# Kernel optimization log

Measured on AMD Instinct MI355X. Metric: run time of the kernel, lower is better.

Reference implementation:

```python
import jax, jax.numpy as jnp
import numpy as np

N_NODES = 50000
N_EDGES = 1600000
N_GRAPHS = 512
HID = 64


def _mlp_params(key, din, dout, scale=0.1):
    k1, k2, k3 = jax.random.split(key, 3)
    return (
        jax.random.normal(k1, (din, HID), jnp.float32) * scale, jnp.zeros((HID,), jnp.float32),
        jax.random.normal(k2, (HID, HID), jnp.float32) * scale, jnp.zeros((HID,), jnp.float32),
        jax.random.normal(k3, (HID, dout), jnp.float32) * scale, jnp.zeros((dout,), jnp.float32),
    )


def _mlp(x, w1, b1, w2, b2, w3, b3, out_act=None):
    h = jax.nn.relu(x @ w1 + b1)
    h = jax.nn.relu(h @ w2 + b2)
    o = h @ w3 + b3
    return o if out_act is None else out_act(o)


def setup_inputs() -> dict:
    key = jax.random.key(0)
    ks = jax.random.split(key, 8)
    nf = jax.random.normal(ks[0], (N_NODES, 1), jnp.float32)
    ef = jax.random.normal(ks[1], (N_EDGES, 1), jnp.float32)
    src = jax.random.randint(ks[2], (N_EDGES,), 0, N_NODES)
    dst = jax.random.randint(ks[3], (N_EDGES,), 0, N_NODES)
    graph_id = jnp.sort(jax.random.randint(ks[4], (N_NODES,), 0, N_GRAPHS))
    e_w1, e_b1, e_w2, e_b2, e_w3, e_b3 = _mlp_params(ks[5], 3, 1)   # edge model: [src_nf, dst_nf, ef] -> msg
    n_w1, n_b1, n_w2, n_b2, n_w3, n_b3 = _mlp_params(ks[6], 2, 1)   # node model: [nf, agg] -> unf
    m_w1, m_b1, m_w2, m_b2, m_w3, m_b3 = _mlp_params(ks[7], 1, 1)   # node-wise MLP with Sigmoid out_act
    return dict(nf=nf, ef=ef, src=src, dst=dst, graph_id=graph_id,
                e_w1=e_w1, e_b1=e_b1, e_w2=e_w2, e_b2=e_b2, e_w3=e_w3, e_b3=e_b3,
                n_w1=n_w1, n_b1=n_b1, n_w2=n_w2, n_b2=n_b2, n_w3=n_w3, n_b3=n_b3,
                m_w1=m_w1, m_b1=m_b1, m_w2=m_w2, m_b2=m_b2, m_w3=m_w3, m_b3=m_b3)


def reference(nf, ef, src, dst, graph_id,
              e_w1, e_b1, e_w2, e_b2, e_w3, e_b3,
              n_w1, n_b1, n_w2, n_b2, n_w3, n_b3,
              m_w1, m_b1, m_w2, m_b2, m_w3, m_b3):
    # MPNN layer: message on edges, sum-aggregate to dst nodes, node update
    em_in = jnp.concatenate([nf[src], nf[dst], ef], axis=-1)          # [E, 3]
    msg = _mlp(em_in, e_w1, e_b1, e_w2, e_b2, e_w3, e_b3)             # [E, 1]
    agg = jax.ops.segment_sum(msg, dst, num_segments=N_NODES)        # [N, 1]
    unf = _mlp(jnp.concatenate([nf, agg], axis=-1),
               n_w1, n_b1, n_w2, n_b2, n_w3, n_b3)                    # [N, 1]
    # node-wise MLP with Sigmoid output activation
    node_out = _mlp(unf, m_w1, m_b1, m_w2, m_b2, m_w3, m_b3,
                    out_act=jax.nn.sigmoid)                           # [N, 1]
    # sum readout per graph, then final sigmoid
    rd = jax.ops.segment_sum(node_out, graph_id, num_segments=N_GRAPHS)  # [G, 1]
    return jax.nn.sigmoid(rd)
```

## Files before the change

kernel.cpp:

```cpp
#include <hip/hip_runtime.h>
#include <math.h>

#define HID 64
#define BKT_SHIFT 13
#define BKT_RANGE 8192
#define CCHUNK 32

typedef __attribute__((ext_vector_type(8))) short short8;
typedef __attribute__((ext_vector_type(4))) float f32x4;
typedef unsigned long long ull;

union FragU {
    uint4 q;
    short8 v;
    uint32_t u[4];
};

__device__ __forceinline__ uint32_t cvt_pk_bf16(float lo, float hi) {
    uint32_t r;
    asm("v_cvt_pk_bf16_f32 %0, %1, %2" : "=v"(r) : "v"(lo), "v"(hi));
    return r;
}
__device__ __forceinline__ unsigned short bf16_of(float v) {
    return (unsigned short)(cvt_pk_bf16(v, 0.f) & 0xFFFFu);
}

__global__ void prep_kernel(
    const float* __restrict__ w1,  const float* __restrict__ b1,  const float* __restrict__ w2,
    const float* __restrict__ nw1, const float* __restrict__ nb1, const float* __restrict__ nw2,
    const float* __restrict__ mw1, const float* __restrict__ mb1, const float* __restrict__ mw2,
    unsigned short* __restrict__ w1x,  unsigned short* __restrict__ w2T,
    unsigned short* __restrict__ nw1x, unsigned short* __restrict__ nw2T,
    unsigned short* __restrict__ mw1x, unsigned short* __restrict__ mw2T)
{
    int t = blockIdx.x * 256 + threadIdx.x;
    if (t < 4096) {
        int j = t >> 6, k = t & 63;
        w2T [t] = bf16_of(w2 [k * HID + j]);
        nw2T[t] = bf16_of(nw2[k * HID + j]);
        mw2T[t] = bf16_of(mw2[k * HID + j]);
    }
    if (t < 512) {
        int j = t >> 3, k = t & 7;
        float ve = k == 0 ? w1[j] : k == 1 ? w1[HID + j] : k == 2 ? w1[2 * HID + j] : k == 3 ? b1[j] : 0.f;
        float vn = k == 0 ? nw1[j] : k == 1 ? nw1[HID + j] : k == 2 ? nb1[j] : 0.f;
        float vm = k == 0 ? mw1[j] : k == 1 ? mb1[j] : 0.f;
        w1x [t] = bf16_of(ve);
        nw1x[t] = bf16_of(vn);
        mw1x[t] = bf16_of(vm);
    }
}

__global__ __launch_bounds__(256, 2) void edge_mfma7_kernel(
    const float* __restrict__ nf, const float* __restrict__ ef,
    const int* __restrict__ src, const int* __restrict__ dst,
    const unsigned short* __restrict__ w1x, const unsigned short* __restrict__ w2T,
    const float* __restrict__ b2, const float* __restrict__ w3, const float* __restrict__ b3,
    uint2* __restrict__ recs, ull* __restrict__ offs,
    float* __restrict__ aggFb, int E, int B, int nbatch, int mode)
{
    __shared__ uint2 tile[4][2][16][16];

    const int tid  = threadIdx.x;
    const int lane = tid & 63;
    const int wid  = tid >> 6;
    const int g    = lane >> 4;
    const int eL   = lane & 15;

    FragU af1[4];
#pragma unroll
    for (int t = 0; t < 4; ++t) {
        uint4 q = *(const uint4*)&w1x[(t * 16 + eL) * 8];
        af1[t].q = (g == 0) ? q : make_uint4(0, 0, 0, 0);
    }
    FragU af2[4][2];
#pragma unroll
    for (int t = 0; t < 4; ++t)
#pragma unroll
        for (int h = 0; h < 2; ++h)
            af2[t][h].q = *(const uint4*)&w2T[(t * 16 + eL) * 64 + h * 32 + g * 8];

    f32x4 b2v4[4], w3v4[4];
#pragma unroll
    for (int t = 0; t < 4; ++t) {
        int j = t * 16 + g * 4;
        b2v4[t] = *(const f32x4*)&b2[j];
        w3v4[t] = *(const f32x4*)&w3[j];
    }
    const float b3c = b3[0];

    int bi   = blockIdx.x;
    if (bi >= nbatch) return;
    int eidx = bi * 256 + tid;
    int ei   = eidx < E ? eidx : E - 1;
    int dcur = dst[ei];
    float a  = nf[src[ei]];
    float b  = nf[dcur];
    float c  = ef[ei];

    for (;;) {
        const int nbi   = bi + gridDim.x;
        const bool hn   = nbi < nbatch;
        const int neidx = hn ? nbi * 256 + tid : eidx;
        const int nei   = neidx < E ? neidx : E - 1;
        const int ns    = src[nei];
        const int nd    = dst[nei];
        const float ncf = ef[nei];

        float na = 0.f, nb = 0.f;
        float mymsg = 0.f;

#pragma unroll
        for (int ph = 0; ph < 2; ++ph) {
#pragma unroll
            for (int ss = 0; ss < 2; ++ss) {
                const int s = 2 * ph + ss;
                float av = __shfl(a, s * 16 + eL);
                float bv = __shfl(b, s * 16 + eL);
                float cv = __shfl(c, s * 16 + eL);
                FragU bin;
                bin.u[0] = (g == 0) ? cvt_pk_bf16(av, bv) : 0u;
                bin.u[1] = (g == 0) ? cvt_pk_bf16(cv, 1.0f) : 0u;
                bin.u[2] = 0u; bin.u[3] = 0u;
#pragma unroll
                for (int t = 0; t < 4; ++t) {
                    f32x4 h4 = __builtin_amdgcn_mfma_f32_16x16x32_bf16(
                        af1[t].v, bin.v, (f32x4){0.f, 0.f, 0.f, 0.f}, 0, 0, 0);
                    uint32_t p0 = cvt_pk_bf16(fmaxf(h4[0], 0.f), fmaxf(h4[1], 0.f));
                    uint32_t p1 = cvt_pk_bf16(fmaxf(h4[2], 0.f), fmaxf(h4[3], 0.f));
                    tile[wid][ss][eL][(4 * t + g) ^ ((eL & 7) << 1)] = make_uint2(p0, p1);
                }
            }

            if (ph == 0) {
                na = nf[ns];
                nb = nf[nd];
            }

            __builtin_amdgcn_s_setprio(1);
#pragma unroll
            for (int ss = 0; ss < 2; ++ss) {
                const int s = 2 * ph + ss;
                const uint4* row = (const uint4*)&tile[wid][ss][eL][0];
                FragU bf0, bf1;
                bf0.q = row[(g)     ^ (eL & 7)];
                bf1.q = row[(4 + g) ^ (eL & 7)];

                float q0, q1, q2, q3;
                {
                    f32x4 ac = __builtin_amdgcn_mfma_f32_16x16x32_bf16(af2[0][0].v, bf0.v, b2v4[0], 0, 0, 0);
                    ac = __builtin_amdgcn_mfma_f32_16x16x32_bf16(af2[0][1].v, bf1.v, ac, 0, 0, 0);
                    q0 = fmaxf(ac[0], 0.f) * w3v4[0][0];
                    q0 = fmaf(fmaxf(ac[1], 0.f), w3v4[0][1], q0);
                    q0 = fmaf(fmaxf(ac[2], 0.f), w3v4[0][2], q0);
                    q0 = fmaf(fmaxf(ac[3], 0.f), w3v4[0][3], q0);
                }
                {
                    f32x4 ac = __builtin_amdgcn_mfma_f32_16x16x32_bf16(af2[1][0].v, bf0.v, b2v4[1], 0, 0, 0);
                    ac = __builtin_amdgcn_mfma_f32_16x16x32_bf16(af2[1][1].v, bf1.v, ac, 0, 0, 0);
                    q1 = fmaxf(ac[0], 0.f) * w3v4[1][0];
                    q1 = fmaf(fmaxf(ac[1], 0.f), w3v4[1][1], q1);
                    q1 = fmaf(fmaxf(ac[2], 0.f), w3v4[1][2], q1);
                    q1 = fmaf(fmaxf(ac[3], 0.f), w3v4[1][3], q1);
                }
                {
                    f32x4 ac = __builtin_amdgcn_mfma_f32_16x16x32_bf16(af2[2][0].v, bf0.v, b2v4[2], 0, 0, 0);
                    ac = __builtin_amdgcn_mfma_f32_16x16x32_bf16(af2[2][1].v, bf1.v, ac, 0, 0, 0);
                    q2 = fmaxf(ac[0], 0.f) * w3v4[2][0];
                    q2 = fmaf(fmaxf(ac[1], 0.f), w3v4[2][1], q2);
                    q2 = fmaf(fmaxf(ac[2], 0.f), w3v4[2][2], q2);
                    q2 = fmaf(fmaxf(ac[3], 0.f), w3v4[2][3], q2);
                }
                {
                    f32x4 ac = __builtin_amdgcn_mfma_f32_16x16x32_bf16(af2[3][0].v, bf0.v, b2v4[3], 0, 0, 0);
                    ac = __builtin_amdgcn_mfma_f32_16x16x32_bf16(af2[3][1].v, bf1.v, ac, 0, 0, 0);
                    q3 = fmaxf(ac[0], 0.f) * w3v4[3][0];
                    q3 = fmaf(fmaxf(ac[1], 0.f), w3v4[3][1], q3);
                    q3 = fmaf(fmaxf(ac[2], 0.f), w3v4[3][2], q3);
                    q3 = fmaf(fmaxf(ac[3], 0.f), w3v4[3][3], q3);
                }
                float p = (q0 + q1) + (q2 + q3);
                p += __shfl_xor(p, 16);
                p += __shfl_xor(p, 32);
                if (s == g) mymsg = p + b3c;
            }
            __builtin_amdgcn_s_setprio(0);
        }

        const bool valid = eidx < E;

        if (mode == 1) {
            if (valid) atomicAdd(&aggFb[dcur], mymsg);
        } else {
            const int bkt = dcur >> BKT_SHIFT;
            const ull lt = (1ull << lane) - 1;
            int myslot = 0;
            int off = 0;
            uint32_t pack_lo = 0, pack_hi = 0;
            for (int bb = 0; bb < B; ++bb) {
                if (bb < 4) pack_lo |= (uint32_t)off << (8 * bb);
                else        pack_hi |= (uint32_t)off << (8 * (bb - 4));
                ull m = __ballot(valid && bkt == bb);
                if (valid && bkt == bb) myslot = off + (int)__popcll(m & lt);
                off += (int)__popcll(m);
            }
            pack_hi |= (uint32_t)off << 24;

            const size_t wgl = (size_t)bi * 4 + wid;
            if (valid) recs[wgl * 64 + myslot] = make_uint2((uint32_t)dcur, __float_as_uint(mymsg));
            if (lane == 0) offs[wgl] = ((ull)pack_hi << 32) | (ull)pack_lo;
        }

        if (!hn) break;
        bi = nbi; eidx = neidx; ei = nei;
        a = na; b = nb; c = ncf; dcur = nd;
    }
}

__global__ __launch_bounds__(256) void bucket_accum_kernel(
    const uint2* __restrict__ recs, const ull* __restrict__ offs,
    float* __restrict__ partial, float* __restrict__ rd, int G, int NW, int B)
{
    __shared__ float acc[BKT_RANGE];

    const int b = blockIdx.x / CCHUNK;
    const int c = blockIdx.x % CCHUNK;

    if (blockIdx.x == 0)
        for (int i = threadIdx.x; i < G; i += 256) rd[i] = 0.f;

    for (int i = threadIdx.x; i < BKT_RANGE; i += 256) acc[i] = 0.f;
    __syncthreads();

    const int wpc = (NW + CCHUNK - 1) / CCHUNK;
    const int w0 = c * wpc;
    const int w1 = (w0 + wpc < NW) ? w0 + wpc : NW;
    const int nb = b + 1;
    const int base_node = b << BKT_SHIFT;

    for (int w = w0 + threadIdx.x; w < w1; w += 256) {
        ull ov = offs[w];
        uint32_t lo = (uint32_t)ov, hi = (uint32_t)(ov >> 32);
        int ob = (int)(((b  < 4) ? (lo >> (8 * b))  : (hi >> (8 * (b  - 4)))) & 0xFF);
        int oe = (int)(((nb < 4) ? (lo >> (8 * nb)) : (hi >> (8 * (nb - 4)))) & 0xFF);
        const uint2* rb = recs + (size_t)w * 64;
        for (int r = ob; r < oe; ++r) {
            uint2 rec = rb[r];
            atomicAdd(&acc[(int)rec.x - base_node], __uint_as_float(rec.y));
        }
    }
    __syncthreads();

    float* pb = partial + ((size_t)b * CCHUNK + c) * BKT_RANGE;
    for (int i = threadIdx.x; i < BKT_RANGE; i += 256) pb[i] = acc[i];
}

__global__ __launch_bounds__(256, 2) void node_mfma4_kernel(
    const float* __restrict__ nf, const float* __restrict__ partial,
    const float* __restrict__ aggFb, int nplanes,
    const int* __restrict__ gid,
    const unsigned short* __restrict__ nw1x, const unsigned short* __restrict__ nw2T,
    const float* __restrict__ nb2, const float* __restrict__ nw3, const float* __restrict__ nb3,
    const unsigned short* __restrict__ mw1x, const unsigned short* __restrict__ mw2T,
    const float* __restrict__ mb2, const float* __restrict__ mw3, const float* __restrict__ mb3,
    float* __restrict__ rd, int N)
{
    __shared__ uint2 tile[4][4][16][16];

    const int tid  = threadIdx.x;
    const int lane = tid & 63;
    const int wid  = tid >> 6;
    const int g    = lane >> 4;
    const int eL   = lane & 15;

    const int idx = blockIdx.x * 256 + tid;
    const int i   = idx < N ? idx : N - 1;
    const float x0 = nf[i];
    const int   gg = gid[i];

    float x1;
    if (nplanes == 1) {
        x1 = aggFb[i];
    } else {
        int bb = i >> BKT_SHIFT, nl = i & (BKT_RANGE - 1);
        const float* p = partial + (size_t)bb * CCHUNK * BKT_RANGE + nl;
        x1 = 0.f;
#pragma unroll 8
        for (int c = 0; c < CCHUNK; ++c) x1 += p[(size_t)c * BKT_RANGE];
    }

    float myunf = 0.f, o = 0.f;

    {
        FragU af1[4], af2[4][2];
        f32x4 b2v4[4], w3v4[4];
#pragma unroll
        for (int t = 0; t < 4; ++t) {
            uint4 q = *(const uint4*)&nw1x[(t * 16 + eL) * 8];
            af1[t].q = (g == 0) ? q : make_uint4(0, 0, 0, 0);
#pragma unroll
            for (int h = 0; h < 2; ++h)
                af2[t][h].q = *(const uint4*)&nw2T[(t * 16 + eL) * 64 + h * 32 + g * 8];
            int j = t * 16 + g * 4;
            b2v4[t] = *(const f32x4*)&nb2[j];
            w3v4[t] = *(const f32x4*)&nw3[j];
        }

#pragma unroll
        for (int s = 0; s < 4; ++s) {
            float av = __shfl(x0, s * 16 + eL);
            float bv = __shfl(x1, s * 16 + eL);
            FragU bin;
            bin.u[0] = (g == 0) ? cvt_pk_bf16(av, bv) : 0u;
            bin.u[1] = (g == 0) ? cvt_pk_bf16(1.0f, 0.f) : 0u;
            bin.u[2] = 0u; bin.u[3] = 0u;
#pragma unroll
            for (int t = 0; t < 4; ++t) {
                f32x4 h4 = __builtin_amdgcn_mfma_f32_16x16x32_bf16(
                    af1[t].v, bin.v, (f32x4){0.f, 0.f, 0.f, 0.f}, 0, 0, 0);
                uint32_t p0 = cvt_pk_bf16(fmaxf(h4[0], 0.f), fmaxf(h4[1], 0.f));
                uint32_t p1 = cvt_pk_bf16(fmaxf(h4[2], 0.f), fmaxf(h4[3], 0.f));
                tile[wid][s][eL][(4 * t + g) ^ ((eL & 7) << 1)] = make_uint2(p0, p1);
            }
        }
#pragma unroll
        for (int s = 0; s < 4; ++s) {
            const uint4* row = (const uint4*)&tile[wid][s][eL][0];
            FragU bf0, bf1;
            bf0.q = row[(g)     ^ (eL & 7)];
            bf1.q = row[(4 + g) ^ (eL & 7)];
            float p = 0.f;
#pragma unroll
            for (int t = 0; t < 4; ++t) {
                f32x4 ac = __builtin_amdgcn_mfma_f32_16x16x32_bf16(af2[t][0].v, bf0.v, b2v4[t], 0, 0, 0);
                ac = __builtin_amdgcn_mfma_f32_16x16x32_bf16(af2[t][1].v, bf1.v, ac, 0, 0, 0);
                p = fmaf(fmaxf(ac[0], 0.f), w3v4[t][0], p);
                p = fmaf(fmaxf(ac[1], 0.f), w3v4[t][1], p);
                p = fmaf(fmaxf(ac[2], 0.f), w3v4[t][2], p);
                p = fmaf(fmaxf(ac[3], 0.f), w3v4[t][3], p);
            }
            p += __shfl_xor(p, 16);
            p += __shfl_xor(p, 32);
            if (s == g) myunf = p + nb3[0];
        }
    }

    {
        FragU af1[4], af2[4][2];
        f32x4 b2v4[4], w3v4[4];
#pragma unroll
        for (int t = 0; t < 4; ++t) {
            uint4 q = *(const uint4*)&mw1x[(t * 16 + eL) * 8];
            af1[t].q = (g == 0) ? q : make_uint4(0, 0, 0, 0);
#pragma unroll
            for (int h = 0; h < 2; ++h)
                af2[t][h].q = *(const uint4*)&mw2T[(t * 16 + eL) * 64 + h * 32 + g * 8];
            int j = t * 16 + g * 4;
            b2v4[t] = *(const f32x4*)&mb2[j];
            w3v4[t] = *(const f32x4*)&mw3[j];
        }

#pragma unroll
        for (int s = 0; s < 4; ++s) {
            float uv = __shfl(myunf, s * 16 + eL);
            FragU bin;
            bin.u[0] = (g == 0) ? cvt_pk_bf16(uv, 1.0f) : 0u;
            bin.u[1] = 0u; bin.u[2] = 0u; bin.u[3] = 0u;
#pragma unroll
            for (int t = 0; t < 4; ++t) {
                f32x4 h4 = __builtin_amdgcn_mfma_f32_16x16x32_bf16(
                    af1[t].v, bin.v, (f32x4){0.f, 0.f, 0.f, 0.f}, 0, 0, 0);
                uint32_t p0 = cvt_pk_bf16(fmaxf(h4[0], 0.f), fmaxf(h4[1], 0.f));
                uint32_t p1 = cvt_pk_bf16(fmaxf(h4[2], 0.f), fmaxf(h4[3], 0.f));
                tile[wid][s][eL][(4 * t + g) ^ ((eL & 7) << 1)] = make_uint2(p0, p1);
            }
        }
#pragma unroll
        for (int s = 0; s < 4; ++s) {
            const uint4* row = (const uint4*)&tile[wid][s][eL][0];
            FragU bf0, bf1;
            bf0.q = row[(g)     ^ (eL & 7)];
            bf1.q = row[(4 + g) ^ (eL & 7)];
            float p = 0.f;
#pragma unroll
            for (int t = 0; t < 4; ++t) {
                f32x4 ac = __builtin_amdgcn_mfma_f32_16x16x32_bf16(af2[t][0].v, bf0.v, b2v4[t], 0, 0, 0);
                ac = __builtin_amdgcn_mfma_f32_16x16x32_bf16(af2[t][1].v, bf1.v, ac, 0, 0, 0);
                p = fmaf(fmaxf(ac[0], 0.f), w3v4[t][0], p);
                p = fmaf(fmaxf(ac[1], 0.f), w3v4[t][1], p);
                p = fmaf(fmaxf(ac[2], 0.f), w3v4[t][2], p);
                p = fmaf(fmaxf(ac[3], 0.f), w3v4[t][3], p);
            }
            p += __shfl_xor(p, 16);
            p += __shfl_xor(p, 32);
            if (s == g) o = p + mb3[0];
        }
    }

    const float node_out = 1.0f / (1.0f + expf(-o));

    {
        const bool ok = idx < N;
        float v = ok ? node_out : 0.0f;
        int ggv = gg;
#pragma unroll
        for (int d = 1; d < 64; d <<= 1) {
            float vup = __shfl_up(v, d);
            int   gup = __shfl_up(ggv, d);
            if (lane >= d && gup == ggv) v += vup;
        }
        int gdn = __shfl_down(ggv, 1);
        bool tail = (lane == 63) || (gdn != ggv);
        if (tail)
            atomicAdd(&rd[ggv], v);
    }
}

__global__ void readout_kernel(const float* __restrict__ rd,
                               float* __restrict__ out, int G)
{
    int g = blockIdx.x * blockDim.x + threadIdx.x;
    if (g < G) out[g] = 1.0f / (1.0f + expf(-rd[g]));
}

extern "C" void kernel_launch(void* const* d_in, const int* in_sizes, int n_in,
                              void* d_out, int out_size, void* d_ws, size_t ws_size,
                              hipStream_t stream)
{
    const float* nf  = (const float*)d_in[0];
    const float* ef  = (const float*)d_in[1];
    const int*   src = (const int*)  d_in[2];
    const int*   dst = (const int*)  d_in[3];
    const int*   gid = (const int*)  d_in[4];

    const float* e_w1 = (const float*)d_in[5];
    const float* e_b1 = (const float*)d_in[6];
    const float* e_w2 = (const float*)d_in[7];
    const float* e_b2 = (const float*)d_in[8];
    const float* e_w3 = (const float*)d_in[9];
    const float* e_b3 = (const float*)d_in[10];

    const float* n_w1 = (const float*)d_in[11];
    const float* n_b1 = (const float*)d_in[12];
    const float* n_w2 = (const float*)d_in[13];
    const float* n_b2 = (const float*)d_in[14];
    const float* n_w3 = (const float*)d_in[15];
    const float* n_b3 = (const float*)d_in[16];

    const float* m_w1 = (const float*)d_in[17];
    const float* m_b1 = (const float*)d_in[18];
    const float* m_w2 = (const float*)d_in[19];
    const float* m_b2 = (const float*)d_in[20];
    const float* m_w3 = (const float*)d_in[21];
    const float* m_b3 = (const float*)d_in[22];

    const int N = in_sizes[0];
    const int E = in_sizes[2];
    const int G = out_size;

    const int nbatch = (E + 255) / 256;
    const int NW = (E + 63) / 64;
    const int B  = (N + BKT_RANGE - 1) / BKT_RANGE;

    size_t wts_b  = 32 * 1024;
    size_t recs_b = (size_t)NW * 64 * sizeof(uint2);
    size_t offs_b = (size_t)NW * sizeof(ull);
    size_t part_b = (size_t)B * CCHUNK * BKT_RANGE * sizeof(float);
    size_t need   = wts_b + recs_b + offs_b + part_b + (size_t)G * sizeof(float);
    bool bucketok = (B <= 8) && (need <= ws_size);

    char* wp = (char*)d_ws;
    unsigned short* w1x  = (unsigned short*)(wp);
    unsigned short* nw1x = (unsigned short*)(wp + 1024);
    unsigned short* mw1x = (unsigned short*)(wp + 2048);
    unsigned short* w2T  = (unsigned short*)(wp + 4096);
    unsigned short* nw2T = (unsigned short*)(wp + 4096 + 8192);
    unsigned short* mw2T = (unsigned short*)(wp + 4096 + 16384);

    float* out = (float*)d_out;

    prep_kernel<<<16, 256, 0, stream>>>(
        e_w1, e_b1, e_w2, n_w1, n_b1, n_w2, m_w1, m_b1, m_w2,
        w1x, w2T, nw1x, nw2T, mw1x, mw2T);

    int egrid = nbatch < 2048 ? nbatch : 2048;

    if (bucketok) {
        uint2* recs    = (uint2*)(wp + wts_b);
        ull*   offs    = (ull*)(wp + wts_b + recs_b);
        float* partial = (float*)(wp + wts_b + recs_b + offs_b);
        float* rd      = (float*)(wp + wts_b + recs_b + offs_b + part_b);

        edge_mfma7_kernel<<<egrid, 256, 0, stream>>>(
            nf, ef, src, dst, w1x, w2T, e_b2, e_w3, e_b3,
            recs, offs, nullptr, E, B, nbatch, 0);

        bucket_accum_kernel<<<B * CCHUNK, 256, 0, stream>>>(
            recs, offs, partial, rd, G, NW, B);

        node_mfma4_kernel<<<(N + 255) / 256, 256, 0, stream>>>(
            nf, partial, nullptr, CCHUNK, gid,
            nw1x, nw2T, n_b2, n_w3, n_b3,
            mw1x, mw2T, m_b2, m_w3, m_b3,
            rd, N);

        readout_kernel<<<(G + 255) / 256, 256, 0, stream>>>(rd, out, G);
    } else {
        float* agg = (float*)(wp + wts_b);
        float* rd  = agg + N;

        hipMemsetAsync(agg, 0, ((size_t)N + G) * sizeof(float), stream);

        edge_mfma7_kernel<<<egrid, 256, 0, stream>>>(
            nf, ef, src, dst, w1x, w2T, e_b2, e_w3, e_b3,
            nullptr, nullptr, agg, E, B, nbatch, 1);

        node_mfma4_kernel<<<(N + 255) / 256, 256, 0, stream>>>(
            nf, nullptr, agg, 1, gid,
            nw1x, nw2T, n_b2, n_w3, n_b3,
            mw1x, mw2T, m_b2, m_w3, m_b3,
            rd, N);

        readout_kernel<<<(G + 255) / 256, 256, 0, stream>>>(rd, out, G);
    }
}
```

Before: 78.41 us.

## Remove prep and readout launches by converting weights in-kernel and fusing readout

Result: faster. 71.94 us, median of 2 (-8.2%).

```diff
diff --git a/kernel.cpp b/kernel.cpp
--- a/kernel.cpp
+++ b/kernel.cpp
@@ -21,45 +21,17 @@
     asm("v_cvt_pk_bf16_f32 %0, %1, %2" : "=v"(r) : "v"(lo), "v"(hi));
     return r;
 }
-__device__ __forceinline__ unsigned short bf16_of(float v) {
-    return (unsigned short)(cvt_pk_bf16(v, 0.f) & 0xFFFFu);
-}
-
-__global__ void prep_kernel(
-    const float* __restrict__ w1,  const float* __restrict__ b1,  const float* __restrict__ w2,
-    const float* __restrict__ nw1, const float* __restrict__ nb1, const float* __restrict__ nw2,
-    const float* __restrict__ mw1, const float* __restrict__ mb1, const float* __restrict__ mw2,
-    unsigned short* __restrict__ w1x,  unsigned short* __restrict__ w2T,
-    unsigned short* __restrict__ nw1x, unsigned short* __restrict__ nw2T,
-    unsigned short* __restrict__ mw1x, unsigned short* __restrict__ mw2T)
-{
-    int t = blockIdx.x * 256 + threadIdx.x;
-    if (t < 4096) {
-        int j = t >> 6, k = t & 63;
-        w2T [t] = bf16_of(w2 [k * HID + j]);
-        nw2T[t] = bf16_of(nw2[k * HID + j]);
-        mw2T[t] = bf16_of(mw2[k * HID + j]);
-    }
-    if (t < 512) {
-        int j = t >> 3, k = t & 7;
-        float ve = k == 0 ? w1[j] : k == 1 ? w1[HID + j] : k == 2 ? w1[2 * HID + j] : k == 3 ? b1[j] : 0.f;
-        float vn = k == 0 ? nw1[j] : k == 1 ? nw1[HID + j] : k == 2 ? nb1[j] : 0.f;
-        float vm = k == 0 ? mw1[j] : k == 1 ? mb1[j] : 0.f;
-        w1x [t] = bf16_of(ve);
-        nw1x[t] = bf16_of(vn);
-        mw1x[t] = bf16_of(vm);
-    }
-}
-
-__global__ __launch_bounds__(256, 2) void edge_mfma7_kernel(
+
+__global__ __launch_bounds__(256, 2) void edge_mfma8_kernel(
     const float* __restrict__ nf, const float* __restrict__ ef,
     const int* __restrict__ src, const int* __restrict__ dst,
-    const unsigned short* __restrict__ w1x, const unsigned short* __restrict__ w2T,
-    const float* __restrict__ b2, const float* __restrict__ w3, const float* __restrict__ b3,
+    const float* __restrict__ w1, const float* __restrict__ b1,
+    const float* __restrict__ w2, const float* __restrict__ b2,
+    const float* __restrict__ w3, const float* __restrict__ b3,
     uint2* __restrict__ recs, ull* __restrict__ offs,
     float* __restrict__ aggFb, int E, int B, int nbatch, int mode)
 {
-    __shared__ uint2 tile[4][2][16][16];
+    __shared__ uint2 tile[4][4][16][16];
 
     const int tid  = threadIdx.x;
     const int lane = tid & 63;
@@ -70,16 +42,24 @@
     FragU af1[4];
 #pragma unroll
     for (int t = 0; t < 4; ++t) {
-        uint4 q = *(const uint4*)&w1x[(t * 16 + eL) * 8];
-        af1[t].q = (g == 0) ? q : make_uint4(0, 0, 0, 0);
+        int j = t * 16 + eL;
+        uint32_t u0 = cvt_pk_bf16(w1[j], w1[HID + j]);
+        uint32_t u1 = cvt_pk_bf16(w1[2 * HID + j], b1[j]);
+        af1[t].u[0] = (g == 0) ? u0 : 0u;
+        af1[t].u[1] = (g == 0) ? u1 : 0u;
+        af1[t].u[2] = 0u; af1[t].u[3] = 0u;
     }
     FragU af2[4][2];
 #pragma unroll
     for (int t = 0; t < 4; ++t)
 #pragma unroll
         for (int h = 0; h < 2; ++h)
-            af2[t][h].q = *(const uint4*)&w2T[(t * 16 + eL) * 64 + h * 32 + g * 8];
-
+#pragma unroll
+            for (int e2 = 0; e2 < 4; ++e2) {
+                int k0 = h * 32 + g * 8 + 2 * e2;
+                int j  = t * 16 + eL;
+                af2[t][h].u[e2] = cvt_pk_bf16(w2[k0 * HID + j], w2[(k0 + 1) * HID + j]);
+            }
     f32x4 b2v4[4], w3v4[4];
 #pragma unroll
     for (int t = 0; t < 4; ++t) {
@@ -97,6 +77,8 @@
     float a  = nf[src[ei]];
     float b  = nf[dcur];
     float c  = ef[ei];
+    uint32_t pkab = cvt_pk_bf16(a, b);
+    uint32_t pkc1 = cvt_pk_bf16(c, 1.0f);
 
     for (;;) {
         const int nbi   = bi + gridDim.x;
@@ -107,84 +89,73 @@
         const int nd    = dst[nei];
         const float ncf = ef[nei];
 
-        float na = 0.f, nb = 0.f;
+#pragma unroll
+        for (int s = 0; s < 4; ++s) {
+            int sel = s * 16 + eL;
+            uint32_t u0 = (uint32_t)__shfl((int)pkab, sel);
+            uint32_t u1 = (uint32_t)__shfl((int)pkc1, sel);
+            FragU bin;
+            bin.u[0] = (g == 0) ? u0 : 0u;
+            bin.u[1] = (g == 0) ? u1 : 0u;
+            bin.u[2] = 0u; bin.u[3] = 0u;
+#pragma unroll
+            for (int t = 0; t < 4; ++t) {
+                f32x4 h4 = __builtin_amdgcn_mfma_f32_16x16x32_bf16(
+                    af1[t].v, bin.v, (f32x4){0.f, 0.f, 0.f, 0.f}, 0, 0, 0);
+                uint32_t p0 = cvt_pk_bf16(fmaxf(h4[0], 0.f), fmaxf(h4[1], 0.f));
+                uint32_t p1 = cvt_pk_bf16(fmaxf(h4[2], 0.f), fmaxf(h4[3], 0.f));
+                tile[wid][s][eL][(4 * t + g) ^ ((eL & 7) << 1)] = make_uint2(p0, p1);
+            }
+        }
+
+        const float na = nf[ns];
+        const float nb = nf[nd];
+
         float mymsg = 0.f;
-
-#pragma unroll
-        for (int ph = 0; ph < 2; ++ph) {
-#pragma unroll
-            for (int ss = 0; ss < 2; ++ss) {
-                const int s = 2 * ph + ss;
-                float av = __shfl(a, s * 16 + eL);
-                float bv = __shfl(b, s * 16 + eL);
-                float cv = __shfl(c, s * 16 + eL);
-                FragU bin;
-                bin.u[0] = (g == 0) ? cvt_pk_bf16(av, bv) : 0u;
-                bin.u[1] = (g == 0) ? cvt_pk_bf16(cv, 1.0f) : 0u;
-                bin.u[2] = 0u; bin.u[3] = 0u;
-#pragma unroll
-                for (int t = 0; t < 4; ++t) {
-                    f32x4 h4 = __builtin_amdgcn_mfma_f32_16x16x32_bf16(
-                        af1[t].v, bin.v, (f32x4){0.f, 0.f, 0.f, 0.f}, 0, 0, 0);
-                    uint32_t p0 = cvt_pk_bf16(fmaxf(h4[0], 0.f), fmaxf(h4[1], 0.f));
-                    uint32_t p1 = cvt_pk_bf16(fmaxf(h4[2], 0.f), fmaxf(h4[3], 0.f));
-                    tile[wid][ss][eL][(4 * t + g) ^ ((eL & 7) << 1)] = make_uint2(p0, p1);
-                }
-            }
-
-            if (ph == 0) {
-                na = nf[ns];
-                nb = nf[nd];
-            }
-
-            __builtin_amdgcn_s_setprio(1);
-#pragma unroll
-            for (int ss = 0; ss < 2; ++ss) {
-                const int s = 2 * ph + ss;
-                const uint4* row = (const uint4*)&tile[wid][ss][eL][0];
-                FragU bf0, bf1;
-                bf0.q = row[(g)     ^ (eL & 7)];
-                bf1.q = row[(4 + g) ^ (eL & 7)];
-
-                float q0, q1, q2, q3;
-                {
-                    f32x4 ac = __builtin_amdgcn_mfma_f32_16x16x32_bf16(af2[0][0].v, bf0.v, b2v4[0], 0, 0, 0);
-                    ac = __builtin_amdgcn_mfma_f32_16x16x32_bf16(af2[0][1].v, bf1.v, ac, 0, 0, 0);
-                    q0 = fmaxf(ac[0], 0.f) * w3v4[0][0];
-                    q0 = fmaf(fmaxf(ac[1], 0.f), w3v4[0][1], q0);
-                    q0 = fmaf(fmaxf(ac[2], 0.f), w3v4[0][2], q0);
-                    q0 = fmaf(fmaxf(ac[3], 0.f), w3v4[0][3], q0);
-                }
-                {
-                    f32x4 ac = __builtin_amdgcn_mfma_f32_16x16x32_bf16(af2[1][0].v, bf0.v, b2v4[1], 0, 0, 0);
-                    ac = __builtin_amdgcn_mfma_f32_16x16x32_bf16(af2[1][1].v, bf1.v, ac, 0, 0, 0);
-                    q1 = fmaxf(ac[0], 0.f) * w3v4[1][0];
-                    q1 = fmaf(fmaxf(ac[1], 0.f), w3v4[1][1], q1);
-                    q1 = fmaf(fmaxf(ac[2], 0.f), w3v4[1][2], q1);
-                    q1 = fmaf(fmaxf(ac[3], 0.f), w3v4[1][3], q1);
-                }
-                {
-                    f32x4 ac = __builtin_amdgcn_mfma_f32_16x16x32_bf16(af2[2][0].v, bf0.v, b2v4[2], 0, 0, 0);
-                    ac = __builtin_amdgcn_mfma_f32_16x16x32_bf16(af2[2][1].v, bf1.v, ac, 0, 0, 0);
-                    q2 = fmaxf(ac[0], 0.f) * w3v4[2][0];
-                    q2 = fmaf(fmaxf(ac[1], 0.f), w3v4[2][1], q2);
-                    q2 = fmaf(fmaxf(ac[2], 0.f), w3v4[2][2], q2);
-                    q2 = fmaf(fmaxf(ac[3], 0.f), w3v4[2][3], q2);
-                }
-                {
-                    f32x4 ac = __builtin_amdgcn_mfma_f32_16x16x32_bf16(af2[3][0].v, bf0.v, b2v4[3], 0, 0, 0);
-                    ac = __builtin_amdgcn_mfma_f32_16x16x32_bf16(af2[3][1].v, bf1.v, ac, 0, 0, 0);
-                    q3 = fmaxf(ac[0], 0.f) * w3v4[3][0];
-                    q3 = fmaf(fmaxf(ac[1], 0.f), w3v4[3][1], q3);
-                    q3 = fmaf(fmaxf(ac[2], 0.f), w3v4[3][2], q3);
-                    q3 = fmaf(fmaxf(ac[3], 0.f), w3v4[3][3], q3);
-                }
-                float p = (q0 + q1) + (q2 + q3);
-                p += __shfl_xor(p, 16);
-                p += __shfl_xor(p, 32);
-                if (s == g) mymsg = p + b3c;
-            }
-            __builtin_amdgcn_s_setprio(0);
+#pragma unroll
+        for (int s = 0; s < 4; ++s) {
+            const uint4* row = (const uint4*)&tile[wid][s][eL][0];
+            FragU bf0, bf1;
+            bf0.q = row[(g)     ^ (eL & 7)];
+            bf1.q = row[(4 + g) ^ (eL & 7)];
+
+            float q0, q1, q2, q3;
+            {
+                f32x4 ac = __builtin_amdgcn_mfma_f32_16x16x32_bf16(af2[0][0].v, bf0.v, b2v4[0], 0, 0, 0);
+                ac = __builtin_amdgcn_mfma_f32_16x16x32_bf16(af2[0][1].v, bf1.v, ac, 0, 0, 0);
+                q0 = fmaxf(ac[0], 0.f) * w3v4[0][0];
+                q0 = fmaf(fmaxf(ac[1], 0.f), w3v4[0][1], q0);
+                q0 = fmaf(fmaxf(ac[2], 0.f), w3v4[0][2], q0);
+                q0 = fmaf(fmaxf(ac[3], 0.f), w3v4[0][3], q0);
+            }
+            {
+                f32x4 ac = __builtin_amdgcn_mfma_f32_16x16x32_bf16(af2[1][0].v, bf0.v, b2v4[1], 0, 0, 0);
+                ac = __builtin_amdgcn_mfma_f32_16x16x32_bf16(af2[1][1].v, bf1.v, ac, 0, 0, 0);
+                q1 = fmaxf(ac[0], 0.f) * w3v4[1][0];
+                q1 = fmaf(fmaxf(ac[1], 0.f), w3v4[1][1], q1);
+                q1 = fmaf(fmaxf(ac[2], 0.f), w3v4[1][2], q1);
+                q1 = fmaf(fmaxf(ac[3], 0.f), w3v4[1][3], q1);
+            }
+            {
+                f32x4 ac = __builtin_amdgcn_mfma_f32_16x16x32_bf16(af2[2][0].v, bf0.v, b2v4[2], 0, 0, 0);
+                ac = __builtin_amdgcn_mfma_f32_16x16x32_bf16(af2[2][1].v, bf1.v, ac, 0, 0, 0);
+                q2 = fmaxf(ac[0], 0.f) * w3v4[2][0];
+                q2 = fmaf(fmaxf(ac[1], 0.f), w3v4[2][1], q2);
+                q2 = fmaf(fmaxf(ac[2], 0.f), w3v4[2][2], q2);
+                q2 = fmaf(fmaxf(ac[3], 0.f), w3v4[2][3], q2);
+            }
+            {
+                f32x4 ac = __builtin_amdgcn_mfma_f32_16x16x32_bf16(af2[3][0].v, bf0.v, b2v4[3], 0, 0, 0);
+                ac = __builtin_amdgcn_mfma_f32_16x16x32_bf16(af2[3][1].v, bf1.v, ac, 0, 0, 0);
+                q3 = fmaxf(ac[0], 0.f) * w3v4[3][0];
+                q3 = fmaf(fmaxf(ac[1], 0.f), w3v4[3][1], q3);
+                q3 = fmaf(fmaxf(ac[2], 0.f), w3v4[3][2], q3);
+                q3 = fmaf(fmaxf(ac[3], 0.f), w3v4[3][3], q3);
+            }
+            float p = (q0 + q1) + (q2 + q3);
+            p += __shfl_xor(p, 16);
+            p += __shfl_xor(p, 32);
+            if (s == g) mymsg = p + b3c;
         }
 
         const bool valid = eidx < E;
@@ -212,22 +183,27 @@
         }
 
         if (!hn) break;
-        bi = nbi; eidx = neidx; ei = nei;
-        a = na; b = nb; c = ncf; dcur = nd;
+        bi = nbi; eidx = neidx;
+        pkab = cvt_pk_bf16(na, nb);
+        pkc1 = cvt_pk_bf16(ncf, 1.0f);
+        dcur = nd;
     }
 }
 
 __global__ __launch_bounds__(256) void bucket_accum_kernel(
     const uint2* __restrict__ recs, const ull* __restrict__ offs,
-    float* __restrict__ partial, float* __restrict__ rd, int G, int NW, int B)
+    float* __restrict__ partial, float* __restrict__ rd, unsigned* __restrict__ ctr,
+    int G, int NW, int B)
 {
     __shared__ float acc[BKT_RANGE];
 
     const int b = blockIdx.x / CCHUNK;
     const int c = blockIdx.x % CCHUNK;
 
-    if (blockIdx.x == 0)
+    if (blockIdx.x == 0) {
         for (int i = threadIdx.x; i < G; i += 256) rd[i] = 0.f;
+        if (threadIdx.x == 0) *ctr = 0u;
+    }
 
     for (int i = threadIdx.x; i < BKT_RANGE; i += 256) acc[i] = 0.f;
     __syncthreads();
@@ -255,17 +231,21 @@
     for (int i = threadIdx.x; i < BKT_RANGE; i += 256) pb[i] = acc[i];
 }
 
-__global__ __launch_bounds__(256, 2) void node_mfma4_kernel(
+__global__ __launch_bounds__(256, 2) void node_mfma5_kernel(
     const float* __restrict__ nf, const float* __restrict__ partial,
     const float* __restrict__ aggFb, int nplanes,
     const int* __restrict__ gid,
-    const unsigned short* __restrict__ nw1x, const unsigned short* __restrict__ nw2T,
-    const float* __restrict__ nb2, const float* __restrict__ nw3, const float* __restrict__ nb3,
-    const unsigned short* __restrict__ mw1x, const unsigned short* __restrict__ mw2T,
-    const float* __restrict__ mb2, const float* __restrict__ mw3, const float* __restrict__ mb3,
-    float* __restrict__ rd, int N)
+    const float* __restrict__ nw1, const float* __restrict__ nb1,
+    const float* __restrict__ nw2, const float* __restrict__ nb2,
+    const float* __restrict__ nw3, const float* __restrict__ nb3,
+    const float* __restrict__ mw1, const float* __restrict__ mb1,
+    const float* __restrict__ mw2, const float* __restrict__ mb2,
+    const float* __restrict__ mw3, const float* __restrict__ mb3,
+    float* __restrict__ rd, float* __restrict__ outp, unsigned* __restrict__ ctr,
+    int N, int G)
 {
     __shared__ uint2 tile[4][4][16][16];
+    __shared__ int lastflag;
 
     const int tid  = threadIdx.x;
     const int lane = tid & 63;
@@ -296,23 +276,33 @@
         f32x4 b2v4[4], w3v4[4];
 #pragma unroll
         for (int t = 0; t < 4; ++t) {
-            uint4 q = *(const uint4*)&nw1x[(t * 16 + eL) * 8];
-            af1[t].q = (g == 0) ? q : make_uint4(0, 0, 0, 0);
+            int j = t * 16 + eL;
+            uint32_t u0 = cvt_pk_bf16(nw1[j], nw1[HID + j]);
+            uint32_t u1 = cvt_pk_bf16(nb1[j], 0.f);
+            af1[t].u[0] = (g == 0) ? u0 : 0u;
+            af1[t].u[1] = (g == 0) ? u1 : 0u;
+            af1[t].u[2] = 0u; af1[t].u[3] = 0u;
 #pragma unroll
             for (int h = 0; h < 2; ++h)
-                af2[t][h].q = *(const uint4*)&nw2T[(t * 16 + eL) * 64 + h * 32 + g * 8];
-            int j = t * 16 + g * 4;
-            b2v4[t] = *(const f32x4*)&nb2[j];
-            w3v4[t] = *(const f32x4*)&nw3[j];
-        }
+#pragma unroll
+                for (int e2 = 0; e2 < 4; ++e2) {
+                    int k0 = h * 32 + g * 8 + 2 * e2;
+                    af2[t][h].u[e2] = cvt_pk_bf16(nw2[k0 * HID + j], nw2[(k0 + 1) * HID + j]);
+                }
+            int j4 = t * 16 + g * 4;
+            b2v4[t] = *(const f32x4*)&nb2[j4];
+            w3v4[t] = *(const f32x4*)&nw3[j4];
+        }
+        uint32_t pk01 = cvt_pk_bf16(x0, x1);
+        uint32_t pkb  = cvt_pk_bf16(1.0f, 0.f);
 
 #pragma unroll
         for (int s = 0; s < 4; ++s) {
-            float av = __shfl(x0, s * 16 + eL);
-            float bv = __shfl(x1, s * 16 + eL);
+            int sel = s * 16 + eL;
+            uint32_t u0 = (uint32_t)__shfl((int)pk01, sel);
             FragU bin;
-            bin.u[0] = (g == 0) ? cvt_pk_bf16(av, bv) : 0u;
-            bin.u[1] = (g == 0) ? cvt_pk_bf16(1.0f, 0.f) : 0u;
+            bin.u[0] = (g == 0) ? u0 : 0u;
+            bin.u[1] = (g == 0) ? pkb : 0u;
             bin.u[2] = 0u; bin.u[3] = 0u;
 #pragma unroll
             for (int t = 0; t < 4; ++t) {
@@ -350,14 +340,20 @@
         f32x4 b2v4[4], w3v4[4];
 #pragma unroll
         for (int t = 0; t < 4; ++t) {
-            uint4 q = *(const uint4*)&mw1x[(t * 16 + eL) * 8];
-            af1[t].q = (g == 0) ? q : make_uint4(0, 0, 0, 0);
+            int j = t * 16 + eL;
+            uint32_t u0 = cvt_pk_bf16(mw1[j], mb1[j]);
+            af1[t].u[0] = (g == 0) ? u0 : 0u;
+            af1[t].u[1] = 0u; af1[t].u[2] = 0u; af1[t].u[3] = 0u;
 #pragma unroll
             for (int h = 0; h < 2; ++h)
-                af2[t][h].q = *(const uint4*)&mw2T[(t * 16 + eL) * 64 + h * 32 + g * 8];
-            int j = t * 16 + g * 4;
-            b2v4[t] = *(const f32x4*)&mb2[j];
-            w3v4[t] = *(const f32x4*)&mw3[j];
+#pragma unroll
+                for (int e2 = 0; e2 < 4; ++e2) {
+                    int k0 = h * 32 + g * 8 + 2 * e2;
+                    af2[t][h].u[e2] = cvt_pk_bf16(mw2[k0 * HID + j], mw2[(k0 + 1) * HID + j]);
+                }
+            int j4 = t * 16 + g * 4;
+            b2v4[t] = *(const f32x4*)&mb2[j4];
+            w3v4[t] = *(const f32x4*)&mw3[j4];
         }
 
 #pragma unroll
@@ -413,6 +409,20 @@
         bool tail = (lane == 63) || (gdn != ggv);
         if (tail)
             atomicAdd(&rd[ggv], v);
+    }
+
+    if (ctr) {
+        if (tid == 0) {
+            __threadfence();
+            unsigned v = atomicAdd(ctr, 1u);
+            lastflag = (v == (unsigned)(gridDim.x - 1)) ? 1 : 0;
+        }
+        __syncthreads();
+        if (lastflag) {
+            __threadfence();
+            for (int q = tid; q < G; q += 256)
+                outp[q] = 1.0f / (1.0f + expf(-rd[q]));
+        }
     }
 }
 
@@ -462,65 +472,52 @@
     const int NW = (E + 63) / 64;
     const int B  = (N + BKT_RANGE - 1) / BKT_RANGE;
 
-    size_t wts_b  = 32 * 1024;
     size_t recs_b = (size_t)NW * 64 * sizeof(uint2);
     size_t offs_b = (size_t)NW * sizeof(ull);
     size_t part_b = (size_t)B * CCHUNK * BKT_RANGE * sizeof(float);
-    size_t need   = wts_b + recs_b + offs_b + part_b + (size_t)G * sizeof(float);
+    size_t need   = recs_b + offs_b + part_b + (size_t)G * sizeof(float) + 64;
     bool bucketok = (B <= 8) && (need <= ws_size);
 
     char* wp = (char*)d_ws;
-    unsigned short* w1x  = (unsigned short*)(wp);
-    unsigned short* nw1x = (unsigned short*)(wp + 1024);
-    unsigned short* mw1x = (unsigned short*)(wp + 2048);
-    unsigned short* w2T  = (unsigned short*)(wp + 4096);
-    unsigned short* nw2T = (unsigned short*)(wp + 4096 + 8192);
-    unsigned short* mw2T = (unsigned short*)(wp + 4096 + 16384);
-
     float* out = (float*)d_out;
 
-    prep_kernel<<<16, 256, 0, stream>>>(
-        e_w1, e_b1, e_w2, n_w1, n_b1, n_w2, m_w1, m_b1, m_w2,
-        w1x, w2T, nw1x, nw2T, mw1x, mw2T);
-
-    int egrid = nbatch < 2048 ? nbatch : 2048;
+    int egrid = nbatch < 1024 ? nbatch : 1024;
 
     if (bucketok) {
-        uint2* recs    = (uint2*)(wp + wts_b);
-        ull*   offs    = (ull*)(wp + wts_b + recs_b);
-        float* partial = (float*)(wp + wts_b + recs_b + offs_b);
-        float* rd      = (float*)(wp + wts_b + recs_b + offs_b + part_b);
-
-        edge_mfma7_kernel<<<egrid, 256, 0, stream>>>(
-            nf, ef, src, dst, w1x, w2T, e_b2, e_w3, e_b3,
+        uint2*    recs    = (uint2*)wp;
+        ull*      offs    = (ull*)(wp + recs_b);
+        float*    partial = (float*)(wp + recs_b + offs_b);
+        float*    rd      = (float*)(wp + recs_b + offs_b + part_b);
+        unsigned* ctr     = (unsigned*)(wp + recs_b + offs_b + part_b + (size_t)G * sizeof(float));
+
+        edge_mfma8_kernel<<<egrid, 256, 0, stream>>>(
+            nf, ef, src, dst, e_w1, e_b1, e_w2, e_b2, e_w3, e_b3,
             recs, offs, nullptr, E, B, nbatch, 0);
 
         bucket_accum_kernel<<<B * CCHUNK, 256, 0, stream>>>(
-            recs, offs, partial, rd, G, NW, B);
-
-        node_mfma4_kernel<<<(N + 255) / 256, 256, 0, stream>>>(
+            recs, offs, partial, rd, ctr, G, NW, B);
+
+        node_mfma5_kernel<<<(N + 255) / 256, 256, 0, stream>>>(
             nf, partial, nullptr, CCHUNK, gid,
-            nw1x, nw2T, n_b2, n_w3, n_b3,
-            mw1x, mw2T, m_b2, m_w3, m_b3,
-            rd, N);
+            n_w1, n_b1, n_w2, n_b2, n_w3, n_b3,
+            m_w1, m_b1, m_w2, m_b2, m_w3, m_b3,
+            rd, out, ctr, N, G);
+    } else {
+        float* agg = (float*)wp;
+        float* rd  = agg + N;
+
+        hipMemsetAsync(agg, 0, ((size_t)N + G) * sizeof(float), stream);
+
+        edge_mfma8_kernel<<<egrid, 256, 0, stream>>>(
+            nf, ef, src, dst, e_w1, e_b1, e_w2, e_b2, e_w3, e_b3,
+            nullptr, nullptr, agg, E, B, nbatch, 1);
+
+        node_mfma5_kernel<<<(N + 255) / 256, 256, 0, stream>>>(
+            nf, nullptr, agg, 1, gid,
+            n_w1, n_b1, n_w2, n_b2, n_w3, n_b3,
+            m_w1, m_b1, m_w2, m_b2, m_w3, m_b3,
+            rd, out, nullptr, N, G);
 
         readout_kernel<<<(G + 255) / 256, 256, 0, stream>>>(rd, out, G);
-    } else {
-        float* agg = (float*)(wp + wts_b);
-        float* rd  = agg + N;
-
-        hipMemsetAsync(agg, 0, ((size_t)N + G) * sizeof(float), stream);
-
-        edge_mfma7_kernel<<<egrid, 256, 0, stream>>>(
-            nf, ef, src, dst, w1x, w2T, e_b2, e_w3, e_b3,
-            nullptr, nullptr, agg, E, B, nbatch, 1);
-
-        node_mfma4_kernel<<<(N + 255) / 256, 256, 0, stream>>>(
-            nf, nullptr, agg, 1, gid,
-            nw1x, nw2T, n_b2, n_w3, n_b3,
-            mw1x, mw2T, m_b2, m_w3, m_b3,
-            rd, N);
-
-        readout_kernel<<<(G + 255) / 256, 256, 0, stream>>>(rd, out, G);
     }
 }
```
